# Kernel optimization log

Measured on AMD Instinct MI355X. Metric: run time of the kernel, lower is better.

## Reference

```python
import jax, jax.numpy as jnp
import numpy as np

ELEMENTS = np.array([1, 6, 7, 8, 16])  # H, C, N, O, S
N_ATOMS = 200_000
N_IN, N_HID, N_ELEM = 256, 128, len(ELEMENTS)


def setup_inputs() -> dict:
    key = jax.random.key(0)
    ks = jax.random.split(key, 6)
    elem_idx = jax.random.randint(ks[0], (N_ATOMS,), 0, N_ELEM)
    atomic_numbers = jnp.asarray(ELEMENTS)[elem_idx].astype(jnp.int64)
    representation = jax.random.normal(ks[1], (N_ATOMS, N_IN), dtype=jnp.float32)
    s1 = 1.0 / np.sqrt(N_IN)
    s2 = 1.0 / np.sqrt(N_HID)
    W1 = jax.random.normal(ks[2], (N_ELEM, N_HID, N_IN), dtype=jnp.float32) * s1
    b1 = jax.random.normal(ks[3], (N_ELEM, N_HID), dtype=jnp.float32) * s1
    W2 = jax.random.normal(ks[4], (N_ELEM, 1, N_HID), dtype=jnp.float32) * s2
    b2 = jax.random.normal(ks[5], (N_ELEM, 1), dtype=jnp.float32) * s2
    return {"atomic_numbers": atomic_numbers, "representation": representation,
            "W1": W1, "b1": b1, "W2": W2, "b2": b2}


def reference(atomic_numbers, representation, W1, b1, W2, b2):
    # All-experts dense compute: hidden [N, E, H]
    h = jax.nn.silu(jnp.einsum('nd,ehd->neh', representation, W1) + b1[None])
    # Output head (n_out = 1): y [N, E]
    y = jnp.einsum('neh,eoh->neo', h, W2)[..., 0] + b2[None, :, 0]
    # One-hot element mask (equivalent to the frozen embedding lookup)
    mask = (atomic_numbers[:, None] == jnp.asarray(ELEMENTS)[None, :]).astype(y.dtype)
    return jnp.sum(y * mask, axis=1, keepdims=True)  # [N, 1]
```

## Files before the change

kernel.cpp:

```cpp
#include <hip/hip_runtime.h>
#include <hip/hip_bf16.h>

#define N_IN    256
#define N_HID   128
#define N_ELEM  5
#define NBLK    512
#define ESTRIDE 66560

typedef __attribute__((ext_vector_type(8))) short  short8;
typedef __attribute__((ext_vector_type(4))) short  short4v;
typedef __attribute__((ext_vector_type(4))) float  float4v;

__device__ __forceinline__ int expert_of(int z) {
    return (z == 1) ? 0 : (z == 6) ? 1 : (z == 7) ? 2 : (z == 8) ? 3 : 4;
}
__device__ __forceinline__ short f2bf(float f) {
    union { float f; unsigned u; } c; c.f = f;
    unsigned r = (c.u + 0x7fffu + ((c.u >> 16) & 1u)) >> 16;
    return (short)r;
}

#define AS3 __attribute__((address_space(3)))
#define GLOAD_LDS16(gsrc, ldst) \
    __builtin_amdgcn_global_load_lds((const __attribute__((address_space(1))) void*)(gsrc), \
                                     (AS3 void*)(ldst), 16, 0, 0)
__device__ __forceinline__ unsigned lds_off(const void* p) {
    return (unsigned)(size_t)(AS3 const char*)p;
}

#define DSR128(dst, a) asm volatile("ds_read_b128 %0, %1" : "=v"(dst) : "v"(a))
#define LGKM0 do { asm volatile("s_waitcnt lgkmcnt(0)" ::: "memory"); \
                   __builtin_amdgcn_sched_barrier(0); } while (0)
#define WAITV0 do { asm volatile("s_waitcnt vmcnt(0)" ::: "memory"); \
                    __builtin_amdgcn_sched_barrier(0); } while (0)

__global__ void prep_hist_kernel(const float* __restrict__ W1, const float* __restrict__ B1f,
                                 const float* __restrict__ W2f, char* __restrict__ W1s,
                                 const int* __restrict__ z, int n, int* __restrict__ counts) {
    if (blockIdx.x < 85) {
        int idx = blockIdx.x * 256 + threadIdx.x;
        if (idx < 20480) {
            int e = idx >> 12, rem = idx & 4095;
            int slot = rem >> 6, lane = rem & 63;
            int nrow = (slot >> 3) * 16 + (lane & 15);
            int k0 = (slot & 7) * 32 + (lane >> 4) * 8;
            const float* src = W1 + ((size_t)(e * N_HID + nrow) * N_IN + k0);
            float4v f0 = *(const float4v*)src;
            float4v f1 = *(const float4v*)(src + 4);
            short8 s;
            s[0] = f2bf(f0[0]); s[1] = f2bf(f0[1]); s[2] = f2bf(f0[2]); s[3] = f2bf(f0[3]);
            s[4] = f2bf(f1[0]); s[5] = f2bf(f1[1]); s[6] = f2bf(f1[2]); s[7] = f2bf(f1[3]);
            *(short8*)(W1s + (size_t)e * ESTRIDE + slot * 1024 + lane * 16) = s;
        } else {
            int idx2 = idx - 20480;
            int e = idx2 >> 8, i = idx2 & 255;
            float* dst = (float*)(W1s + (size_t)e * ESTRIDE + 65536);
            if (i < 128) dst[i] = B1f[e * N_HID + i];
            else         dst[128 + (i - 128)] = W2f[e * N_HID + (i - 128)];
        }
        return;
    }
    __shared__ int cnt[N_ELEM];
    if (threadIdx.x < N_ELEM) cnt[threadIdx.x] = 0;
    __syncthreads();
    int i = (blockIdx.x - 85) * blockDim.x + threadIdx.x;
    if (i < n) atomicAdd(&cnt[expert_of(z[i])], 1);
    __syncthreads();
    if (threadIdx.x < N_ELEM && cnt[threadIdx.x]) atomicAdd(&counts[threadIdx.x], cnt[threadIdx.x]);
}

__global__ void scatter_kernel(const int* __restrict__ z, int n,
                               const int* __restrict__ counts,
                               int* __restrict__ cursorRel, int* __restrict__ perm) {
    __shared__ int cnt[N_ELEM], cur[N_ELEM], base[N_ELEM];
    int tid = threadIdx.x;
    if (tid < N_ELEM) { cnt[tid] = 0; cur[tid] = 0; }
    __syncthreads();
    int i = blockIdx.x * blockDim.x + tid;
    int e = -1;
    if (i < n) { e = expert_of(z[i]); atomicAdd(&cnt[e], 1); }
    __syncthreads();
    if (tid < N_ELEM) {
        int pfx = 0;
        for (int k = 0; k < tid; ++k) pfx += counts[k];
        base[tid] = cnt[tid] ? pfx + atomicAdd(&cursorRel[tid], cnt[tid]) : 0;
    }
    __syncthreads();
    if (e >= 0) {
        int r = atomicAdd(&cur[e], 1);
        perm[base[e] + r] = i;
    }
}

__launch_bounds__(256, 2)
__global__ void mlp_kernel(const float* __restrict__ X, const char* __restrict__ W1s,
                           const float* __restrict__ B2f, const int* __restrict__ perm,
                           const int* __restrict__ counts, float* __restrict__ out) {
    __shared__ char Bs[65536];

    int lane = threadIdx.x & 63;
    int w    = threadIdx.x >> 6;
    int am   = lane & 15, g = lane >> 4;

    int cntv[N_ELEM], so[N_ELEM], ns[N_ELEM];
    int nSub = 0, acc0 = 0;
#pragma unroll
    for (int e = 0; e < N_ELEM; ++e) {
        cntv[e] = counts[e];
        so[e] = acc0; acc0 += cntv[e];
        ns[e] = (cntv[e] + 15) >> 4;
        nSub += ns[e];
    }
    int blk[N_ELEM], tot = 0;
#pragma unroll
    for (int e = 0; e < N_ELEM; ++e) {
        blk[e] = (int)(((long long)NBLK * ns[e]) / nSub);
        tot += blk[e];
    }
    int rem = NBLK - tot;
#pragma unroll
    for (int e = 0; e < N_ELEM; ++e)
        if (rem > 0 && ns[e] > 0) { blk[e]++; rem--; }
    while (rem > 0) { blk[0]++; rem--; }
#pragma unroll
    for (int e = 0; e < N_ELEM; ++e)
        if (ns[e] > 0 && blk[e] == 0) {
            int m = 0;
            for (int j = 1; j < N_ELEM; ++j) if (blk[j] > blk[m]) m = j;
            blk[m]--; blk[e]++;
        }
    int bp1 = blk[0], bp2 = bp1 + blk[1], bp3 = bp2 + blk[2], bp4 = bp3 + blk[3];

    int b = blockIdx.x;
    int e = (b >= bp1) + (b >= bp2) + (b >= bp3) + (b >= bp4);
    int bloc = b - ((e == 0) ? 0 : (e == 1) ? bp1 : (e == 2) ? bp2 : (e == 3) ? bp3 : bp4);
    int BE = blk[e], NE = ns[e];
    int soE = so[e], ctE = cntv[e];

    const char* img = W1s + (size_t)e * ESTRIDE;
    {
        const char* wsrc = img + w * 16384 + lane * 16;
        char* wdst = Bs + w * 16384;
#pragma unroll
        for (int i = 0; i < 16; ++i)
            GLOAD_LDS16(wsrc + i * 1024, wdst + i * 1024);
    }
    WAITV0;
    __syncthreads();

    int qe = (BE > 0) ? NE / BE : 0, re = (BE > 0) ? NE % BE : 0;
    int tb0 = bloc * qe + min(bloc, re);
    int tb1 = tb0 + qe + (bloc < re ? 1 : 0);
    int L = tb1 - tb0;
    int qw = L >> 2, rw = L & 3;
    int s0 = tb0 + w * qw + min(w, rw);
    int s1 = s0 + qw + (w < rw ? 1 : 0);
    if (s0 >= s1) return;

    unsigned BOFF = lds_off(Bs);
    int lastA = soE + ctE - 1;

    const float* prm = (const float*)(img + 65536);
    float b1c[8], w2c[8];
#pragma unroll
    for (int n = 0; n < 8; ++n) {
        b1c[n] = prm[n * 16 + am];
        w2c[n] = prm[128 + n * 16 + am];
    }
    float b2v = B2f[e];

#define ROWSOF(s_) min(16, ctE - (s_) * 16)
#define GIDOF(s_) perm[min(soE + (s_) * 16 + am, lastA)]

    int rowsC = ROWSOF(s0);
    int gidC = GIDOF(s0);
    float4v rawA[16];
    {
        const float* base0 = X + ((size_t)(unsigned)gidC << 8) + g * 8;
#pragma unroll
        for (int kk = 0; kk < 8; ++kk) {
            rawA[2 * kk]     = *(const float4v*)(base0 + kk * 32);
            rawA[2 * kk + 1] = *(const float4v*)(base0 + kk * 32 + 4);
        }
    }
    int rowsN = rowsC, gidN = gidC;
    if (s0 + 1 < s1) { rowsN = ROWSOF(s0 + 1); gidN = GIDOF(s0 + 1); }

    for (int s = s0; s < s1; ++s) {
        bool pf = (s + 1 < s1);
        const float* baseN = X + ((size_t)(unsigned)gidN << 8) + g * 8;

        float4v acc[8] = {};
#pragma unroll
        for (int kk = 0; kk < 8; ++kk) {
            short8 bpre[8];
#pragma unroll
            for (int n = 0; n < 8; ++n)
                DSR128(bpre[n], BOFF + (unsigned)((n * 8 + kk) * 1024 + lane * 16));
            short8 abf;
            {
                float4v f0 = rawA[2 * kk], f1 = rawA[2 * kk + 1];
                union { __hip_bfloat162 h[4]; short8 v; } u;
                u.h[0] = __float22bfloat162_rn({f0[0], f0[1]});
                u.h[1] = __float22bfloat162_rn({f0[2], f0[3]});
                u.h[2] = __float22bfloat162_rn({f1[0], f1[1]});
                u.h[3] = __float22bfloat162_rn({f1[2], f1[3]});
                abf = u.v;
            }
            if (pf) {
                rawA[2 * kk]     = *(const float4v*)(baseN + kk * 32);
                rawA[2 * kk + 1] = *(const float4v*)(baseN + kk * 32 + 4);
            }
            LGKM0;
#pragma unroll
            for (int n = 0; n < 8; ++n)
                acc[n] = __builtin_amdgcn_mfma_f32_16x16x32_bf16(
                    abf, bpre[n], acc[n], 0, 0, 0);
        }

        float pv0 = 0, pv1 = 0, pv2 = 0, pv3 = 0;
#pragma unroll
        for (int n = 0; n < 8; ++n) {
            float v0 = acc[n][0] + b1c[n]; v0 = v0 / (1.0f + __expf(-v0));
            float v1 = acc[n][1] + b1c[n]; v1 = v1 / (1.0f + __expf(-v1));
            float v2 = acc[n][2] + b1c[n]; v2 = v2 / (1.0f + __expf(-v2));
            float v3 = acc[n][3] + b1c[n]; v3 = v3 / (1.0f + __expf(-v3));
            pv0 += v0 * w2c[n]; pv1 += v1 * w2c[n];
            pv2 += v2 * w2c[n]; pv3 += v3 * w2c[n];
        }
#pragma unroll
        for (int sh = 1; sh <= 8; sh <<= 1) {
            pv0 += __shfl_xor(pv0, sh, 64);
            pv1 += __shfl_xor(pv1, sh, 64);
            pv2 += __shfl_xor(pv2, sh, 64);
            pv3 += __shfl_xor(pv3, sh, 64);
        }
        float val = (am == 0) ? pv0 : (am == 1) ? pv1 : (am == 2) ? pv2 : pv3;
        int tgt = __shfl(gidC, g * 4 + am, 64);
        if (am < 4 && g * 4 + am < rowsC) out[tgt] = val + b2v;

        rowsC = rowsN; gidC = gidN;
        if (s + 2 < s1) { rowsN = ROWSOF(s + 2); gidN = GIDOF(s + 2); }
    }
#undef ROWSOF
#undef GIDOF
}

extern "C" void kernel_launch(void* const* d_in, const int* in_sizes, int n_in,
                              void* d_out, int out_size, void* d_ws, size_t ws_size,
                              hipStream_t stream) {
    const int*   z  = (const int*)  d_in[0];
    const float* X  = (const float*)d_in[1];
    const float* W1 = (const float*)d_in[2];
    const float* B1 = (const float*)d_in[3];
    const float* W2 = (const float*)d_in[4];
    const float* B2 = (const float*)d_in[5];
    float* out = (float*)d_out;
    int nAtoms = in_sizes[0];

    char* ws = (char*)d_ws;
    size_t off = 0;
    char* W1s      = ws + off;         off += (size_t)N_ELEM * ESTRIDE;
    int* perm      = (int*)(ws + off); off += (size_t)nAtoms * 4;
    int* counts    = (int*)(ws + off); off += 32;
    int* cursorRel = (int*)(ws + off); off += 32;

    hipMemsetAsync(counts, 0, 64, stream);

    int hb = (nAtoms + 255) / 256;
    prep_hist_kernel<<<85 + hb, 256, 0, stream>>>(W1, B1, W2, W1s, z, nAtoms, counts);
    scatter_kernel<<<hb, 256, 0, stream>>>(z, nAtoms, counts, cursorRel, perm);
    mlp_kernel<<<NBLK, 256, 0, stream>>>(X, W1s, B2, perm, counts, out);
}
```

Before: 72.02 us.

## Merge prep, histogram and scatter into one cooperative kernel with grid sync

```diff
diff --git a/kernel.cpp b/kernel.cpp
--- a/kernel.cpp
+++ b/kernel.cpp
@@ -1,10 +1,12 @@
 #include <hip/hip_runtime.h>
+#include <hip/hip_cooperative_groups.h>
 #include <hip/hip_bf16.h>
 
 #define N_IN    256
 #define N_HID   128
 #define N_ELEM  5
 #define NBLK    512
+#define PREPB   256
 #define ESTRIDE 66560
 
 typedef __attribute__((ext_vector_type(8))) short  short8;
@@ -34,62 +36,92 @@
 #define WAITV0 do { asm volatile("s_waitcnt vmcnt(0)" ::: "memory"); \
                     __builtin_amdgcn_sched_barrier(0); } while (0)
 
-__global__ void prep_hist_kernel(const float* __restrict__ W1, const float* __restrict__ B1f,
+__global__ void coop_prep_kernel(const float* __restrict__ W1, const float* __restrict__ B1f,
                                  const float* __restrict__ W2f, char* __restrict__ W1s,
-                                 const int* __restrict__ z, int n, int* __restrict__ counts) {
-    if (blockIdx.x < 85) {
-        int idx = blockIdx.x * 256 + threadIdx.x;
-        if (idx < 20480) {
-            int e = idx >> 12, rem = idx & 4095;
-            int slot = rem >> 6, lane = rem & 63;
-            int nrow = (slot >> 3) * 16 + (lane & 15);
-            int k0 = (slot & 7) * 32 + (lane >> 4) * 8;
-            const float* src = W1 + ((size_t)(e * N_HID + nrow) * N_IN + k0);
-            float4v f0 = *(const float4v*)src;
-            float4v f1 = *(const float4v*)(src + 4);
-            short8 s;
-            s[0] = f2bf(f0[0]); s[1] = f2bf(f0[1]); s[2] = f2bf(f0[2]); s[3] = f2bf(f0[3]);
-            s[4] = f2bf(f1[0]); s[5] = f2bf(f1[1]); s[6] = f2bf(f1[2]); s[7] = f2bf(f1[3]);
-            *(short8*)(W1s + (size_t)e * ESTRIDE + slot * 1024 + lane * 16) = s;
-        } else {
-            int idx2 = idx - 20480;
-            int e = idx2 >> 8, i = idx2 & 255;
-            float* dst = (float*)(W1s + (size_t)e * ESTRIDE + 65536);
-            if (i < 128) dst[i] = B1f[e * N_HID + i];
-            else         dst[128 + (i - 128)] = W2f[e * N_HID + (i - 128)];
-        }
-        return;
-    }
-    __shared__ int cnt[N_ELEM];
-    if (threadIdx.x < N_ELEM) cnt[threadIdx.x] = 0;
-    __syncthreads();
-    int i = (blockIdx.x - 85) * blockDim.x + threadIdx.x;
-    if (i < n) atomicAdd(&cnt[expert_of(z[i])], 1);
-    __syncthreads();
-    if (threadIdx.x < N_ELEM && cnt[threadIdx.x]) atomicAdd(&counts[threadIdx.x], cnt[threadIdx.x]);
-}
-
-__global__ void scatter_kernel(const int* __restrict__ z, int n,
-                               const int* __restrict__ counts,
-                               int* __restrict__ cursorRel, int* __restrict__ perm) {
-    __shared__ int cnt[N_ELEM], cur[N_ELEM], base[N_ELEM];
-    int tid = threadIdx.x;
-    if (tid < N_ELEM) { cnt[tid] = 0; cur[tid] = 0; }
-    __syncthreads();
-    int i = blockIdx.x * blockDim.x + tid;
-    int e = -1;
-    if (i < n) { e = expert_of(z[i]); atomicAdd(&cnt[e], 1); }
-    __syncthreads();
-    if (tid < N_ELEM) {
-        int pfx = 0;
-        for (int k = 0; k < tid; ++k) pfx += counts[k];
-        base[tid] = cnt[tid] ? pfx + atomicAdd(&cursorRel[tid], cnt[tid]) : 0;
-    }
-    __syncthreads();
-    if (e >= 0) {
-        int r = atomicAdd(&cur[e], 1);
-        perm[base[e] + r] = i;
-    }
+                                 const int* __restrict__ z, int n,
+                                 int* __restrict__ blockCnt, int* __restrict__ counts,
+                                 int* __restrict__ perm) {
+    namespace cg = cooperative_groups;
+    cg::grid_group grid = cg::this_grid();
+
+    __shared__ int cntL[N_ELEM];
+    __shared__ int baseL[N_ELEM];
+    __shared__ int redT[4][N_ELEM], redP[4][N_ELEM];
+
+    int tid  = threadIdx.x;
+    int b    = blockIdx.x;
+    int gtid = b * 256 + tid;
+    int w    = tid >> 6, lane = tid & 63;
+
+    if (tid < N_ELEM) cntL[tid] = 0;
+    __syncthreads();
+
+    if (gtid < 20480) {
+        int e = gtid >> 12, rem = gtid & 4095;
+        int slot = rem >> 6, ln = rem & 63;
+        int nrow = (slot >> 3) * 16 + (ln & 15);
+        int k0 = (slot & 7) * 32 + (ln >> 4) * 8;
+        const float* src = W1 + ((size_t)(e * N_HID + nrow) * N_IN + k0);
+        float4v f0 = *(const float4v*)src;
+        float4v f1 = *(const float4v*)(src + 4);
+        short8 s;
+        s[0] = f2bf(f0[0]); s[1] = f2bf(f0[1]); s[2] = f2bf(f0[2]); s[3] = f2bf(f0[3]);
+        s[4] = f2bf(f1[0]); s[5] = f2bf(f1[1]); s[6] = f2bf(f1[2]); s[7] = f2bf(f1[3]);
+        *(short8*)(W1s + (size_t)e * ESTRIDE + slot * 1024 + ln * 16) = s;
+    } else if (gtid < 21760) {
+        int idx2 = gtid - 20480;
+        int e = idx2 >> 8, i = idx2 & 255;
+        float* dst = (float*)(W1s + (size_t)e * ESTRIDE + 65536);
+        if (i < 128) dst[i] = B1f[e * N_HID + i];
+        else         dst[128 + (i - 128)] = W2f[e * N_HID + (i - 128)];
+    }
+
+    int eR[4], rR[4], aR[4];
+#pragma unroll
+    for (int k = 0; k < 4; ++k) {
+        int a = gtid + k * 65536;
+        aR[k] = a; eR[k] = -1; rR[k] = 0;
+        if (a < n) {
+            eR[k] = expert_of(z[a]);
+            rR[k] = atomicAdd(&cntL[eR[k]], 1);
+        }
+    }
+    __syncthreads();
+    if (tid < N_ELEM) blockCnt[b * N_ELEM + tid] = cntL[tid];
+
+    grid.sync();
+
+    int v[N_ELEM];
+#pragma unroll
+    for (int e = 0; e < N_ELEM; ++e) v[e] = blockCnt[tid * N_ELEM + e];
+    int fl = (tid < b) ? 1 : 0;
+#pragma unroll
+    for (int e = 0; e < N_ELEM; ++e) {
+        int s = v[e], p = fl ? v[e] : 0;
+#pragma unroll
+        for (int sh = 1; sh <= 32; sh <<= 1) {
+            s += __shfl_xor(s, sh, 64);
+            p += __shfl_xor(p, sh, 64);
+        }
+        if (lane == 0) { redT[w][e] = s; redP[w][e] = p; }
+    }
+    __syncthreads();
+    if (tid == 0) {
+        int seg = 0;
+#pragma unroll
+        for (int e = 0; e < N_ELEM; ++e) {
+            int tot = redT[0][e] + redT[1][e] + redT[2][e] + redT[3][e];
+            int pre = redP[0][e] + redP[1][e] + redP[2][e] + redP[3][e];
+            baseL[e] = seg + pre;
+            if (b == 0) counts[e] = tot;
+            seg += tot;
+        }
+    }
+    __syncthreads();
+
+#pragma unroll
+    for (int k = 0; k < 4; ++k)
+        if (eR[k] >= 0) perm[baseL[eR[k]] + rR[k]] = aR[k];
 }
 
 __launch_bounds__(256, 2)
@@ -260,15 +292,16 @@
 
     char* ws = (char*)d_ws;
     size_t off = 0;
-    char* W1s      = ws + off;         off += (size_t)N_ELEM * ESTRIDE;
-    int* perm      = (int*)(ws + off); off += (size_t)nAtoms * 4;
-    int* counts    = (int*)(ws + off); off += 32;
-    int* cursorRel = (int*)(ws + off); off += 32;
-
-    hipMemsetAsync(counts, 0, 64, stream);
-
-    int hb = (nAtoms + 255) / 256;
-    prep_hist_kernel<<<85 + hb, 256, 0, stream>>>(W1, B1, W2, W1s, z, nAtoms, counts);
-    scatter_kernel<<<hb, 256, 0, stream>>>(z, nAtoms, counts, cursorRel, perm);
+    char* W1s     = ws + off;          off += (size_t)N_ELEM * ESTRIDE;
+    int* perm     = (int*)(ws + off);  off += (size_t)nAtoms * 4;
+    int* counts   = (int*)(ws + off);  off += 32;
+    int* blockCnt = (int*)(ws + off);  off += (size_t)PREPB * N_ELEM * 4;
+
+    void* args[] = {(void*)&W1, (void*)&B1, (void*)&W2, (void*)&W1s,
+                    (void*)&z, (void*)&nAtoms, (void*)&blockCnt,
+                    (void*)&counts, (void*)&perm};
+    hipLaunchCooperativeKernel((const void*)coop_prep_kernel,
+                               dim3(PREPB), dim3(256), args, 0, stream);
+
     mlp_kernel<<<NBLK, 256, 0, stream>>>(X, W1s, B2, perm, counts, out);
 }
```

Result: slower. 85.28 us (+18.4%).

## Replace atomic histogram and scatter with per-block counts and ballot ranks

Applied to the files above, without the earlier changes.

```diff
diff --git a/kernel.cpp b/kernel.cpp
--- a/kernel.cpp
+++ b/kernel.cpp
@@ -36,7 +36,8 @@
 
 __global__ void prep_hist_kernel(const float* __restrict__ W1, const float* __restrict__ B1f,
                                  const float* __restrict__ W2f, char* __restrict__ W1s,
-                                 const int* __restrict__ z, int n, int* __restrict__ counts) {
+                                 const int* __restrict__ z, int n,
+                                 int* __restrict__ blockCnt) {
     if (blockIdx.x < 85) {
         int idx = blockIdx.x * 256 + threadIdx.x;
         if (idx < 20480) {
@@ -51,7 +52,7 @@
             s[0] = f2bf(f0[0]); s[1] = f2bf(f0[1]); s[2] = f2bf(f0[2]); s[3] = f2bf(f0[3]);
             s[4] = f2bf(f1[0]); s[5] = f2bf(f1[1]); s[6] = f2bf(f1[2]); s[7] = f2bf(f1[3]);
             *(short8*)(W1s + (size_t)e * ESTRIDE + slot * 1024 + lane * 16) = s;
-        } else {
+        } else if (idx < 21760) {
             int idx2 = idx - 20480;
             int e = idx2 >> 8, i = idx2 & 255;
             float* dst = (float*)(W1s + (size_t)e * ESTRIDE + 65536);
@@ -60,36 +61,81 @@
         }
         return;
     }
-    __shared__ int cnt[N_ELEM];
-    if (threadIdx.x < N_ELEM) cnt[threadIdx.x] = 0;
-    __syncthreads();
-    int i = (blockIdx.x - 85) * blockDim.x + threadIdx.x;
-    if (i < n) atomicAdd(&cnt[expert_of(z[i])], 1);
-    __syncthreads();
-    if (threadIdx.x < N_ELEM && cnt[threadIdx.x]) atomicAdd(&counts[threadIdx.x], cnt[threadIdx.x]);
-}
-
-__global__ void scatter_kernel(const int* __restrict__ z, int n,
-                               const int* __restrict__ counts,
-                               int* __restrict__ cursorRel, int* __restrict__ perm) {
-    __shared__ int cnt[N_ELEM], cur[N_ELEM], base[N_ELEM];
-    int tid = threadIdx.x;
-    if (tid < N_ELEM) { cnt[tid] = 0; cur[tid] = 0; }
-    __syncthreads();
-    int i = blockIdx.x * blockDim.x + tid;
-    int e = -1;
-    if (i < n) { e = expert_of(z[i]); atomicAdd(&cnt[e], 1); }
+    __shared__ int wcnt[4][N_ELEM];
+    int b = blockIdx.x - 85;
+    int tid = threadIdx.x, w = tid >> 6, lane = tid & 63;
+    int a = b * 256 + tid;
+    int e = (a < n) ? expert_of(z[a]) : -1;
+#pragma unroll
+    for (int ex = 0; ex < N_ELEM; ++ex) {
+        unsigned long long m = __ballot(e == ex);
+        if (lane == 0) wcnt[w][ex] = __popcll(m);
+    }
+    __syncthreads();
+    if (tid < N_ELEM)
+        blockCnt[b * N_ELEM + tid] =
+            wcnt[0][tid] + wcnt[1][tid] + wcnt[2][tid] + wcnt[3][tid];
+}
+
+__global__ void scatter_kernel(const int* __restrict__ z, int n, int nb,
+                               const int* __restrict__ blockCnt,
+                               int* __restrict__ counts, int* __restrict__ perm) {
+    __shared__ int wcnt[4][N_ELEM], wbase[4][N_ELEM];
+    __shared__ int redT[4][N_ELEM], redB[4][N_ELEM];
+    __shared__ int blockBase[N_ELEM];
+
+    int tid = threadIdx.x, b = blockIdx.x;
+    int w = tid >> 6, lane = tid & 63;
+    int a = b * 256 + tid;
+    int e = (a < n) ? expert_of(z[a]) : -1;
+
+    int rankInWave = 0;
+#pragma unroll
+    for (int ex = 0; ex < N_ELEM; ++ex) {
+        unsigned long long m = __ballot(e == ex);
+        if (e == ex) rankInWave = __popcll(m & ((1ull << lane) - 1ull));
+        if (lane == 0) wcnt[w][ex] = __popcll(m);
+    }
     __syncthreads();
     if (tid < N_ELEM) {
-        int pfx = 0;
-        for (int k = 0; k < tid; ++k) pfx += counts[k];
-        base[tid] = cnt[tid] ? pfx + atomicAdd(&cursorRel[tid], cnt[tid]) : 0;
-    }
-    __syncthreads();
-    if (e >= 0) {
-        int r = atomicAdd(&cur[e], 1);
-        perm[base[e] + r] = i;
-    }
+        int s = 0;
+#pragma unroll
+        for (int ww = 0; ww < 4; ++ww) { wbase[ww][tid] = s; s += wcnt[ww][tid]; }
+    }
+
+    int tot[N_ELEM] = {}, below[N_ELEM] = {};
+    for (int idx = tid; idx < nb; idx += 256) {
+        int isb = (idx < b);
+#pragma unroll
+        for (int ex = 0; ex < N_ELEM; ++ex) {
+            int v = blockCnt[idx * N_ELEM + ex];
+            tot[ex] += v;
+            below[ex] += isb ? v : 0;
+        }
+    }
+#pragma unroll
+    for (int ex = 0; ex < N_ELEM; ++ex) {
+#pragma unroll
+        for (int sh = 1; sh <= 32; sh <<= 1) {
+            tot[ex]   += __shfl_xor(tot[ex], sh, 64);
+            below[ex] += __shfl_xor(below[ex], sh, 64);
+        }
+        if (lane == 0) { redT[w][ex] = tot[ex]; redB[w][ex] = below[ex]; }
+    }
+    __syncthreads();
+    if (tid == 0) {
+        int seg = 0;
+#pragma unroll
+        for (int ex = 0; ex < N_ELEM; ++ex) {
+            int T  = redT[0][ex] + redT[1][ex] + redT[2][ex] + redT[3][ex];
+            int Bl = redB[0][ex] + redB[1][ex] + redB[2][ex] + redB[3][ex];
+            blockBase[ex] = seg + Bl;
+            if (b == 0) counts[ex] = T;
+            seg += T;
+        }
+    }
+    __syncthreads();
+    if (e >= 0) perm[blockBase[e] + wbase[w][e] + rankInWave] = a;
 }
 
 __launch_bounds__(256, 2)
@@ -258,17 +304,16 @@
     float* out = (float*)d_out;
     int nAtoms = in_sizes[0];
 
+    int hb = (nAtoms + 255) / 256;
+
     char* ws = (char*)d_ws;
     size_t off = 0;
-    char* W1s      = ws + off;         off += (size_t)N_ELEM * ESTRIDE;
-    int* perm      = (int*)(ws + off); off += (size_t)nAtoms * 4;
-    int* counts    = (int*)(ws + off); off += 32;
-    int* cursorRel = (int*)(ws + off); off += 32;
-
-    hipMemsetAsync(counts, 0, 64, stream);
-
-    int hb = (nAtoms + 255) / 256;
-    prep_hist_kernel<<<85 + hb, 256, 0, stream>>>(W1, B1, W2, W1s, z, nAtoms, counts);
-    scatter_kernel<<<hb, 256, 0, stream>>>(z, nAtoms, counts, cursorRel, perm);
+    char* W1s     = ws + off;          off += (size_t)N_ELEM * ESTRIDE;
+    int* perm     = (int*)(ws + off);  off += (size_t)nAtoms * 4;
+    int* counts   = (int*)(ws + off);  off += 32;
+    int* blockCnt = (int*)(ws + off);  off += (size_t)hb * N_ELEM * 4;
+
+    prep_hist_kernel<<<85 + hb, 256, 0, stream>>>(W1, B1, W2, W1s, z, nAtoms, blockCnt);
+    scatter_kernel<<<hb, 256, 0, stream>>>(z, nAtoms, hb, blockCnt, counts, perm);
     mlp_kernel<<<NBLK, 256, 0, stream>>>(X, W1s, B2, perm, counts, out);
 }
```

Result: faster. 57.63 us (-20.0%).
